# Kernel tuning notes

Hardware: AMD Instinct MI355X
Metric: run time of the kernel (lower is better)

## Reference

```python
import jax, jax.numpy as jnp
import numpy as np


def reference(key, value, time_decay, time_first):
    # key, value: [B, T, H]; time_decay/time_first: [H]
    u = time_first
    w = -jnp.exp(time_decay)
    B, T, H = key.shape

    def step(carry, kv):
        a, b, exponent = carry  # each [B, H]
        kt, vt = kv             # [B, H] each
        # numerically stabilized WKV output at this timestep
        max_e = jnp.maximum(exponent, u + kt)
        wt = jnp.exp(u + kt - max_e)
        scale = jnp.exp(exponent - max_e)
        wkv = (a * scale + wt * vt) / (b * scale + wt)
        # state update with decay w
        max_e2 = jnp.maximum(exponent + w, kt)
        s1 = jnp.exp(exponent + w - max_e2)
        s2 = jnp.exp(kt - max_e2)
        a_new = s1 * a + s2 * vt
        b_new = s1 * b + s2
        return (a_new, b_new, max_e2), wkv

    init = (
        jnp.zeros((B, H), dtype=key.dtype),
        jnp.zeros((B, H), dtype=key.dtype),
        jnp.full((B, H), -jnp.inf, dtype=key.dtype),
    )
    k_t = jnp.transpose(key, (1, 0, 2))    # [T, B, H]
    v_t = jnp.transpose(value, (1, 0, 2))  # [T, B, H]
    _, out = jax.lax.scan(step, init, (k_t, v_t))
    return jnp.transpose(out, (1, 0, 2))   # [B, T, H]


def setup_inputs() -> dict:
    k = jax.random.key(0)
    k1, k2, k3, k4 = jax.random.split(k, 4)
    B, T, H = 8, 2048, 768
    return {
        "key": jax.random.normal(k1, (B, T, H), dtype=jnp.float32),
        "value": jax.random.normal(k2, (B, T, H), dtype=jnp.float32),
        "time_decay": jax.random.normal(k3, (H,), dtype=jnp.float32),
        "time_first": jax.random.normal(k4, (H,), dtype=jnp.float32),
    }
```

## Files before the change

### kernel.cpp

```cpp
#include <hip/hip_runtime.h>
#include <math.h>


#define B_  8
#define T_  2048
#define H_  768
#define NC_ 32
#define L_  64

__global__ __launch_bounds__(256) void wkv_phase1(
    const float* __restrict__ key, const float* __restrict__ val,
    const float* __restrict__ time_decay,
    float* __restrict__ wa, float* __restrict__ wb, float* __restrict__ we)
{
    const int h = blockIdx.x * 256 + threadIdx.x;
    const int c = blockIdx.y;
    const int b = blockIdx.z;

    const float w = -__expf(time_decay[h]);

    const size_t base = ((size_t)b * T_ + (size_t)c * L_) * H_ + h;
    const float* kp = key + base;
    const float* vp = val + base;

    float a = 0.f, bb = 0.f, e = -INFINITY;
#pragma unroll 4
    for (int t = 0; t < L_; ++t) {
        const float kt = kp[(size_t)t * H_];
        const float vt = vp[(size_t)t * H_];
        const float ew = e + w;
        const float m2 = fmaxf(ew, kt);
        const float s1 = __expf(ew - m2);
        const float s2 = __expf(kt - m2);
        a  = fmaf(s1, a,  s2 * vt);
        bb = fmaf(s1, bb, s2);
        e  = m2;
    }
    const size_t off = ((size_t)b * NC_ + c) * H_ + h;
    wa[off] = a; wb[off] = bb; we[off] = e;
}

__global__ __launch_bounds__(256) void wkv_phase2(
    float* __restrict__ wa, float* __restrict__ wb, float* __restrict__ we,
    const float* __restrict__ time_decay)
{
    const int idx = blockIdx.x * 256 + threadIdx.x;
    const int b = idx / H_;
    const int h = idx - b * H_;

    const float wL = -__expf(time_decay[h]) * (float)L_;

    float ra = 0.f, rb = 0.f, re = -INFINITY;

    size_t off = (size_t)b * NC_ * H_ + h;
    float ca = wa[off], cb = wb[off], ce = we[off];

#pragma unroll
    for (int c = 0; c < NC_; ++c) {
        const size_t noff = off + H_;
        float na = 0.f, nb = 0.f, ne = 0.f;
        if (c + 1 < NC_) {
            na = wa[noff]; nb = wb[noff]; ne = we[noff];
        }
        wa[off] = ra; wb[off] = rb; we[off] = re;

        const float e1 = re + wL;
        const float m  = fmaxf(e1, ce);
        const float p  = __expf(e1 - m);
        const float q  = __expf(ce - m);
        ra = fmaf(ra, p, ca * q);
        rb = fmaf(rb, p, cb * q);
        re = m;

        ca = na; cb = nb; ce = ne;
        off = noff;
    }
}

__global__ __launch_bounds__(256) void wkv_phase3(
    const float* __restrict__ key, const float* __restrict__ val,
    const float* __restrict__ time_decay, const float* __restrict__ time_first,
    const float* __restrict__ wa, const float* __restrict__ wb,
    const float* __restrict__ we, float* __restrict__ out)
{
    const int h = blockIdx.x * 256 + threadIdx.x;
    const int c = blockIdx.y;
    const int b = blockIdx.z;

    const float u = time_first[h];
    const float w = -__expf(time_decay[h]);

    const size_t soff = ((size_t)b * NC_ + c) * H_ + h;
    float a  = wa[soff];
    float bb = wb[soff];
    float e  = we[soff];

    const size_t base = ((size_t)b * T_ + (size_t)c * L_) * H_ + h;
    const float* kp = key + base;
    const float* vp = val + base;
    float*       op = out + base;

#pragma unroll 4
    for (int t = 0; t < L_; ++t) {
        const float kt = kp[(size_t)t * H_];
        const float vt = vp[(size_t)t * H_];

        const float uk = u + kt;
        const float m1 = fmaxf(e, uk);
        const float wt = __expf(uk - m1);
        const float sc = __expf(e - m1);
        const float num = fmaf(a,  sc, wt * vt);
        const float den = fmaf(bb, sc, wt);
        op[(size_t)t * H_] = num / den;

        const float ew = e + w;
        const float m2 = fmaxf(ew, kt);
        const float s1 = __expf(ew - m2);
        const float s2 = __expf(kt - m2);
        a  = fmaf(s1, a,  s2 * vt);
        bb = fmaf(s1, bb, s2);
        e  = m2;
    }
}

extern "C" void kernel_launch(void* const* d_in, const int* in_sizes, int n_in,
                              void* d_out, int out_size, void* d_ws, size_t ws_size,
                              hipStream_t stream) {
    const float* key = (const float*)d_in[0];
    const float* val = (const float*)d_in[1];
    const float* td  = (const float*)d_in[2];
    const float* tf  = (const float*)d_in[3];
    float* out = (float*)d_out;

    float* wa = (float*)d_ws;
    float* wb = wa + (size_t)B_ * NC_ * H_;
    float* we = wb + (size_t)B_ * NC_ * H_;

    dim3 blk(256);
    dim3 grid13(H_ / 256, NC_, B_);
    wkv_phase1<<<grid13, blk, 0, stream>>>(key, val, td, wa, wb, we);

    dim3 grid2((B_ * H_) / 256);
    wkv_phase2<<<grid2, blk, 0, stream>>>(wa, wb, we, td);

    wkv_phase3<<<grid13, blk, 0, stream>>>(key, val, td, tf, wa, wb, we, out);
}
```

Baseline: 161.8 us.

## Fuse three WKV phases into one kernel with shared-memory chunk scan

```diff
diff --git a/kernel.cpp b/kernel.cpp
--- a/kernel.cpp
+++ b/kernel.cpp
@@ -7,17 +7,26 @@
 #define H_  768
 #define NC_ 32
 #define L_  64
+#define HG_ 32
+#define NT_ (NC_ * HG_)
 
-__global__ __launch_bounds__(256) void wkv_phase1(
+__global__ __launch_bounds__(NT_) void wkv_fused(
     const float* __restrict__ key, const float* __restrict__ val,
-    const float* __restrict__ time_decay,
-    float* __restrict__ wa, float* __restrict__ wb, float* __restrict__ we)
+    const float* __restrict__ time_decay, const float* __restrict__ time_first,
+    float* __restrict__ out)
 {
-    const int h = blockIdx.x * 256 + threadIdx.x;
-    const int c = blockIdx.y;
-    const int b = blockIdx.z;
+    __shared__ float sa[2][NC_][HG_];
+    __shared__ float sb[2][NC_][HG_];
+    __shared__ float se[2][NC_][HG_];
+
+    const int tid = threadIdx.x;
+    const int c   = tid >> 5;
+    const int ho  = tid & 31;
+    const int h   = blockIdx.x * HG_ + ho;
+    const int b   = blockIdx.y;
 
     const float w = -__expf(time_decay[h]);
+    const float u = time_first[h];
 
     const size_t base = ((size_t)b * T_ + (size_t)c * L_) * H_ + h;
     const float* kp = key + base;
@@ -36,90 +45,64 @@
         bb = fmaf(s1, bb, s2);
         e  = m2;
     }
-    const size_t off = ((size_t)b * NC_ + c) * H_ + h;
-    wa[off] = a; wb[off] = bb; we[off] = e;
-}
 
-__global__ __launch_bounds__(256) void wkv_phase2(
-    float* __restrict__ wa, float* __restrict__ wb, float* __restrict__ we,
-    const float* __restrict__ time_decay)
-{
-    const int idx = blockIdx.x * 256 + threadIdx.x;
-    const int b = idx / H_;
-    const int h = idx - b * H_;
+    int cur = 0;
+    sa[cur][c][ho] = a; sb[cur][c][ho] = bb; se[cur][c][ho] = e;
+    __syncthreads();
 
-    const float wL = -__expf(time_decay[h]) * (float)L_;
+    const float wL = w * (float)L_;
+#pragma unroll
+    for (int s = 0; s < 5; ++s) {
+        const int d = 1 << s;
+        float na = sa[cur][c][ho];
+        float nb = sb[cur][c][ho];
+        float ne = se[cur][c][ho];
+        if (c >= d) {
+            const float pa = sa[cur][c - d][ho];
+            const float pb = sb[cur][c - d][ho];
+            const float pe = se[cur][c - d][ho] + wL * (float)d;
+            const float m  = fmaxf(pe, ne);
+            const float x  = __expf(pe - m);
+            const float y  = __expf(ne - m);
+            na = fmaf(pa, x, na * y);
+            nb = fmaf(pb, x, nb * y);
+            ne = m;
+        }
+        sa[cur ^ 1][c][ho] = na;
+        sb[cur ^ 1][c][ho] = nb;
+        se[cur ^ 1][c][ho] = ne;
+        __syncthreads();
+        cur ^= 1;
+    }
 
     float ra = 0.f, rb = 0.f, re = -INFINITY;
+    if (c > 0) {
+        ra = sa[cur][c - 1][ho];
+        rb = sb[cur][c - 1][ho];
+        re = se[cur][c - 1][ho];
+    }
 
-    size_t off = (size_t)b * NC_ * H_ + h;
-    float ca = wa[off], cb = wb[off], ce = we[off];
-
-#pragma unroll
-    for (int c = 0; c < NC_; ++c) {
-        const size_t noff = off + H_;
-        float na = 0.f, nb = 0.f, ne = 0.f;
-        if (c + 1 < NC_) {
-            na = wa[noff]; nb = wb[noff]; ne = we[noff];
-        }
-        wa[off] = ra; wb[off] = rb; we[off] = re;
-
-        const float e1 = re + wL;
-        const float m  = fmaxf(e1, ce);
-        const float p  = __expf(e1 - m);
-        const float q  = __expf(ce - m);
-        ra = fmaf(ra, p, ca * q);
-        rb = fmaf(rb, p, cb * q);
-        re = m;
-
-        ca = na; cb = nb; ce = ne;
-        off = noff;
-    }
-}
-
-__global__ __launch_bounds__(256) void wkv_phase3(
-    const float* __restrict__ key, const float* __restrict__ val,
-    const float* __restrict__ time_decay, const float* __restrict__ time_first,
-    const float* __restrict__ wa, const float* __restrict__ wb,
-    const float* __restrict__ we, float* __restrict__ out)
-{
-    const int h = blockIdx.x * 256 + threadIdx.x;
-    const int c = blockIdx.y;
-    const int b = blockIdx.z;
-
-    const float u = time_first[h];
-    const float w = -__expf(time_decay[h]);
-
-    const size_t soff = ((size_t)b * NC_ + c) * H_ + h;
-    float a  = wa[soff];
-    float bb = wb[soff];
-    float e  = we[soff];
-
-    const size_t base = ((size_t)b * T_ + (size_t)c * L_) * H_ + h;
-    const float* kp = key + base;
-    const float* vp = val + base;
-    float*       op = out + base;
-
+    float* op = out + base;
 #pragma unroll 4
     for (int t = 0; t < L_; ++t) {
         const float kt = kp[(size_t)t * H_];
         const float vt = vp[(size_t)t * H_];
 
         const float uk = u + kt;
-        const float m1 = fmaxf(e, uk);
+        const float m1 = fmaxf(re, uk);
         const float wt = __expf(uk - m1);
-        const float sc = __expf(e - m1);
-        const float num = fmaf(a,  sc, wt * vt);
-        const float den = fmaf(bb, sc, wt);
+        const float sc = __expf(re - m1);
+        const float num = fmaf(ra, sc, wt * vt);
+        const float den = fmaf(rb, sc, wt);
         op[(size_t)t * H_] = num / den;
 
-        const float ew = e + w;
+        const float ew = re + w;
         const float m2 = fmaxf(ew, kt);
         const float s1 = __expf(ew - m2);
         const float s2 = __expf(kt - m2);
-        a  = fmaf(s1, a,  s2 * vt);
-        bb = fmaf(s1, bb, s2);
-        e  = m2;
+        ra = fmaf(s1, ra, s2 * vt);
+        rb = fmaf(s1, rb, s2);
+        re = m2;
     }
 }
 
@@ -132,16 +115,6 @@
     const float* tf  = (const float*)d_in[3];
     float* out = (float*)d_out;
 
-    float* wa = (float*)d_ws;
-    float* wb = wa + (size_t)B_ * NC_ * H_;
-    float* we = wb + (size_t)B_ * NC_ * H_;
-
-    dim3 blk(256);
-    dim3 grid13(H_ / 256, NC_, B_);
-    wkv_phase1<<<grid13, blk, 0, stream>>>(key, val, td, wa, wb, we);
-
-    dim3 grid2((B_ * H_) / 256);
-    wkv_phase2<<<grid2, blk, 0, stream>>>(wa, wb, we, td);
-
-    wkv_phase3<<<grid13, blk, 0, stream>>>(key, val, td, tf, wa, wb, we, out);
+    dim3 grid(H_ / HG_, B_);
+    wkv_fused<<<grid, NT_, 0, stream>>>(key, val, td, tf, out);
 }
```

After: 165.5 us. +2.2%, slower.
